# Kernel optimization log

Measured on AMD Instinct MI355X. Metric: run time of the kernel, lower is better.

Reference implementation:

```python
import jax, jax.numpy as jnp
import numpy as np

EPS = 1e-5

def conv(x, w, b, pad):
    y = jax.lax.conv_general_dilated(x, w, (1, 1), [(pad, pad), (pad, pad)],
                                     dimension_numbers=('NCHW', 'OIHW', 'NCHW'))
    return y + b[None, :, None, None]

def bn(x, g, be, m, v):
    return g[None, :, None, None] * (x - m[None, :, None, None]) * jax.lax.rsqrt(v[None, :, None, None] + EPS) + be[None, :, None, None]

def haar_dwt2(x):
    # pywt db1 dwt2 on even-sized images: per 2x2 block [[a,b],[c,d]]
    # cA=(a+b+c+d)/2, cH=(a+b-c-d)/2, cV=(a-b+c-d)/2, cD=(a-b-c+d)/2
    B, C, H, W = x.shape
    xr = x.reshape(B, C, H // 2, 2, W // 2, 2)
    a = xr[:, :, :, 0, :, 0]; b = xr[:, :, :, 0, :, 1]
    c = xr[:, :, :, 1, :, 0]; d = xr[:, :, :, 1, :, 1]
    cA = (a + b + c + d) * 0.5
    cH = (a + b - c - d) * 0.5
    cV = (a - b + c - d) * 0.5
    cD = (a - b - c + d) * 0.5
    return jnp.stack([cA, cH, cV, cD], axis=2)  # [B,C,4,H/2,W/2]

def setup_inputs() -> dict:
    key = jax.random.key(0)
    ks = iter(jax.random.split(key, 64))
    def w(shape, s=0.05):
        return jax.random.normal(next(ks), shape, dtype=jnp.float32) * s
    def vecs(c):  # gamma, beta, running_mean, running_var
        return (w((c,), 0.1) + 1.0, w((c,), 0.1), w((c,), 0.1),
                jax.random.uniform(next(ks), (c,), dtype=jnp.float32) + 0.5)
    inp = {'x': jax.random.normal(next(ks), (16, 3, 512, 512), dtype=jnp.float32)}
    inp['cw1'] = w((16, 3, 1, 1)); inp['cb1'] = w((16,))
    inp['cw2'] = w((3, 16, 1, 1)); inp['cb2'] = w((3,))
    inp['lw1'] = w((64, 3, 3, 3)); inp['lb1'] = w((64,))
    inp['lg1'], inp['lbe1'], inp['lm1'], inp['lv1'] = vecs(64)
    inp['lw2'] = w((128, 64, 3, 3)); inp['lb2'] = w((128,))
    inp['lg2'], inp['lbe2'], inp['lm2'], inp['lv2'] = vecs(128)
    inp['hw1'] = w((64, 9, 3, 3)); inp['hb1'] = w((64,))
    inp['hg1'], inp['hbe1'], inp['hm1'], inp['hv1'] = vecs(64)
    inp['hw2'] = w((128, 64, 3, 3)); inp['hb2'] = w((128,))
    inp['hg2'], inp['hbe2'], inp['hm2'], inp['hv2'] = vecs(128)
    inp['fw1'] = w((128, 256, 1, 1)); inp['fb1'] = w((128,))
    inp['fg1'], inp['fbe1'], inp['fm1'], inp['fv1'] = vecs(128)
    inp['fw2'] = w((64, 128, 1, 1)); inp['fb2'] = w((64,))
    inp['fg2'], inp['fbe2'], inp['fm2'], inp['fv2'] = vecs(64)
    return inp

def reference(x, cw1, cb1, cw2, cb2,
              lw1, lb1, lg1, lbe1, lm1, lv1, lw2, lb2, lg2, lbe2, lm2, lv2,
              hw1, hb1, hg1, hbe1, hm1, hv1, hw2, hb2, hg2, hbe2, hm2, hv2,
              fw1, fb1, fg1, fbe1, fm1, fv1, fw2, fb2, fg2, fbe2, fm2, fv2):
    hsv = conv(jax.nn.relu(conv(x, cw1, cb1, 0)), cw2, cb2, 0)
    coeffs = haar_dwt2(hsv)  # [B,3,4,H/2,W/2]
    B, C, _, H, W = coeffs.shape
    low = coeffs[:, :, 0]                                   # [B,3,H,W]
    high = coeffs[:, :, 1:].reshape(B, C * 3, H, W)         # [B,9,H,W]
    lf = jax.nn.relu(bn(conv(low, lw1, lb1, 1), lg1, lbe1, lm1, lv1))
    lf = jax.nn.relu(bn(conv(lf, lw2, lb2, 1), lg2, lbe2, lm2, lv2))
    hf = jax.nn.relu(bn(conv(high, hw1, hb1, 1), hg1, hbe1, hm1, hv1))
    hf = jax.nn.relu(bn(conv(hf, hw2, hb2, 1), hg2, hbe2, hm2, hv2))
    f = jnp.concatenate([lf, hf], axis=1)                   # [B,256,H,W]
    f = jax.nn.relu(bn(conv(f, fw1, fb1, 0), fg1, fbe1, fm1, fv1))
    f = jax.nn.relu(bn(conv(f, fw2, fb2, 0), fg2, fbe2, fm2, fv2))
    return f
```

## Files before the change

### kernel.cpp

```cpp
#include <hip/hip_runtime.h>
#include <hip/hip_bf16.h>


#define EPS_BN 1e-5f

typedef unsigned int u32;
typedef unsigned short u16;
typedef __attribute__((ext_vector_type(8))) short short8;
typedef __attribute__((ext_vector_type(4))) float f32x4;

__device__ __forceinline__ u16 f2bf(float f) {
  u32 u = __float_as_uint(f);
  u32 r = (u + 0x7fffu + ((u >> 16) & 1u)) >> 16;
  return (u16)r;
}

__global__ __launch_bounds__(256) void repack_kernel(
    const float* __restrict__ w, const float* __restrict__ bias,
    const float* __restrict__ g, const float* __restrict__ be,
    const float* __restrict__ m, const float* __restrict__ v,
    float* __restrict__ wrep, float* __restrict__ brep, int K, int COUT)
{
  int idx = blockIdx.x * 256 + threadIdx.x;
  if (idx < K * COUT) {
    int oc = idx % COUT;
    int k  = idx / COUT;
    float alpha = g[oc] * rsqrtf(v[oc] + EPS_BN);
    wrep[idx] = w[(size_t)oc * K + k] * alpha;
  }
  if (idx < COUT) {
    float alpha = g[idx] * rsqrtf(v[idx] + EPS_BN);
    brep[idx] = fmaf(bias[idx], alpha, be[idx] - m[idx] * alpha);
  }
}

__global__ __launch_bounds__(256) void repack_pack_kernel(
    const float* __restrict__ w, const float* __restrict__ bias,
    const float* __restrict__ g, const float* __restrict__ be,
    const float* __restrict__ m, const float* __restrict__ v,
    u16* __restrict__ wpk, float* __restrict__ brep,
    int CIN, int KHW, int COUT)
{
  int idx = blockIdx.x * 256 + threadIdx.x;
  int K = CIN * KHW * KHW;
  if (idx < K * COUT) {
    int oc = idx % COUT;
    int k  = idx / COUT;
    int ic = k % CIN;
    int kidx = k / CIN;
    int ky = kidx / KHW, kx = kidx % KHW;
    float alpha = g[oc] * rsqrtf(v[oc] + EPS_BN);
    float val = w[(((size_t)oc * CIN + ic) * KHW + ky) * KHW + kx] * alpha;
    int ks = k >> 5, c = (k >> 3) & 3, e = k & 7;
    wpk[((size_t)((ks * 4 + c) * COUT + oc)) * 8 + e] = f2bf(val);
  }
  if (idx < COUT) {
    float alpha = g[idx] * rsqrtf(v[idx] + EPS_BN);
    brep[idx] = fmaf(bias[idx], alpha, be[idx] - m[idx] * alpha);
  }
}

__global__ __launch_bounds__(256) void front_kernel(
    const float* __restrict__ x,
    const float* __restrict__ cw1, const float* __restrict__ cb1,
    const float* __restrict__ cw2, const float* __restrict__ cb2,
    float* __restrict__ low, float* __restrict__ high)
{
  const int pid = blockIdx.x * 256 + threadIdx.x;
  const int wo = pid & 255, ho = (pid >> 8) & 255, b = pid >> 16;
  float hsv[2][2][3];
  #pragma unroll
  for (int dy = 0; dy < 2; ++dy) {
    #pragma unroll
    for (int dx = 0; dx < 2; ++dx) {
      int h = 2 * ho + dy, w = 2 * wo + dx;
      size_t base = ((size_t)(b * 3) << 18) + (size_t)h * 512 + w;
      float p0 = x[base];
      float p1 = x[base + (1u << 18)];
      float p2 = x[base + (2u << 18)];
      float o0 = cb2[0], o1 = cb2[1], o2 = cb2[2];
      #pragma unroll
      for (int o = 0; o < 16; ++o) {
        float t = fmaf(cw1[o*3+2], p2, fmaf(cw1[o*3+1], p1, fmaf(cw1[o*3+0], p0, cb1[o])));
        t = fmaxf(t, 0.f);
        o0 = fmaf(cw2[o],      t, o0);
        o1 = fmaf(cw2[16 + o], t, o1);
        o2 = fmaf(cw2[32 + o], t, o2);
      }
      hsv[dy][dx][0] = o0; hsv[dy][dx][1] = o1; hsv[dy][dx][2] = o2;
    }
  }
  size_t lb = (size_t)pid * 3;
  size_t hb = (size_t)pid * 9;
  #pragma unroll
  for (int c = 0; c < 3; ++c) {
    float a  = hsv[0][0][c], bb = hsv[0][1][c];
    float cc = hsv[1][0][c], dd = hsv[1][1][c];
    low [lb + c]         = (a + bb + cc + dd) * 0.5f;
    high[hb + c*3 + 0]   = (a + bb - cc - dd) * 0.5f;
    high[hb + c*3 + 1]   = (a - bb + cc - dd) * 0.5f;
    high[hb + c*3 + 2]   = (a - bb - cc + dd) * 0.5f;
  }
}

template<int CIN, int COUT>
__global__ __launch_bounds__(256, 1) void conv3x3_bn_relu(
    const float* __restrict__ in_, const float* __restrict__ wrep,
    const float* __restrict__ brep, u16* __restrict__ out, int out_stride)
{
  __shared__ __align__(16) float tile[CIN * 18 * 19];
  const int tid = threadIdx.x;
  const int tx = tid & 15, ty = tid >> 4;
  const int w0 = blockIdx.x * 16, h0 = blockIdx.y * 16, b = blockIdx.z;

  for (int idx = tid; idx < 18 * 18 * CIN; idx += 256) {
    int ic = idx % CIN;
    int t  = idx / CIN;
    int x  = t % 18, y = t / 18;
    int gy = h0 + y - 1, gx = w0 + x - 1;
    bool ok = (gy >= 0 && gy < 256 && gx >= 0 && gx < 256);
    size_t gaddr = (size_t)((b * 256 + gy) * 256 + gx) * CIN + ic;
    tile[(ic * 18 + y) * 19 + x] = ok ? in_[gaddr] : 0.f;
  }
  __syncthreads();

  const size_t pix = (size_t)((b * 256 + (h0 + ty)) * 256 + (w0 + tx));
  constexpr int NG = COUT / 16;
  for (int gr = 0; gr < NG; ++gr) {
    float acc[16];
    #pragma unroll
    for (int j = 0; j < 16; ++j) acc[j] = 0.f;
    for (int ic = 0; ic < CIN; ++ic) {
      #pragma unroll
      for (int ky = 0; ky < 3; ++ky) {
        #pragma unroll
        for (int kx = 0; kx < 3; ++kx) {
          float a = tile[(ic * 18 + (ty + ky)) * 19 + (tx + kx)];
          const float* wp = wrep + (size_t)(ic * 9 + ky * 3 + kx) * COUT + gr * 16;
          #pragma unroll
          for (int j = 0; j < 16; ++j) acc[j] = fmaf(a, wp[j], acc[j]);
        }
      }
    }
    const float* bp = brep + gr * 16;
    size_t obase = pix * (size_t)out_stride + gr * 16;
    #pragma unroll
    for (int j = 0; j < 16; ++j) {
      float r = fmaxf(acc[j] + bp[j], 0.f);
      out[obase + j] = f2bf(r);
    }
  }
}

__global__ __launch_bounds__(256, 2) void conv3x3_mfma(
    const u16* __restrict__ in, const u16* __restrict__ wpk,
    const float* __restrict__ brep, u16* __restrict__ out,
    int out_stride, int out_choff)
{
  __shared__ __align__(16) unsigned char smem[3 * 8 * 132 * 16];
  uint4 (*Arow)[8][132] = (uint4(*)[8][132])smem;

  const int tid = threadIdx.x;
  const int l = tid & 63, wid = tid >> 6;
  const int bid = blockIdx.x;
  const int swz = (bid & 7) * 1024 + (bid >> 3);
  const int xh = swz & 1, h = (swz >> 1) & 255, b = swz >> 9;
  const int w0 = xh * 128;

  const int waveM = wid >> 1, waveN = wid & 1;
  const int pixW = waveM * 64, n0 = waveN * 64;
  const int lr = l & 15, lc = l >> 4;

  for (int i = tid; i < 3 * 130 * 8; i += 256) {
    int c = i & 7;
    int t = i >> 3;
    int px = t % 130;
    int row = t / 130;
    int gy = h + row - 1, gx = w0 + px - 1;
    uint4 vv = make_uint4(0, 0, 0, 0);
    if ((unsigned)gy < 256u && (unsigned)gx < 256u)
      vv = *(const uint4*)(in + ((size_t)((b * 256 + gy) * 256 + gx)) * 64 + c * 8);
    Arow[row][c][px] = vv;
  }
  __syncthreads();

  f32x4 acc[4][4];
  #pragma unroll
  for (int m = 0; m < 4; ++m)
    #pragma unroll
    for (int n = 0; n < 4; ++n)
      #pragma unroll
      for (int j = 0; j < 4; ++j) acc[m][n][j] = 0.f;

  const short8* wpk8 = (const short8*)wpk;
  #pragma unroll
  for (int kidx = 0; kidx < 9; ++kidx) {
    const int ky = kidx / 3, kx = kidx % 3;
    #pragma unroll
    for (int cs = 0; cs < 2; ++cs) {
      short8 a[4], bf[4];
      #pragma unroll
      for (int m = 0; m < 4; ++m)
        a[m] = *(const short8*)&Arow[ky][cs * 4 + lc][pixW + m * 16 + lr + kx];
      #pragma unroll
      for (int n = 0; n < 4; ++n)
        bf[n] = wpk8[((kidx * 2 + cs) * 4 + lc) * 128 + n0 + n * 16 + lr];
      #pragma unroll
      for (int m = 0; m < 4; ++m)
        #pragma unroll
        for (int n = 0; n < 4; ++n)
          acc[m][n] = __builtin_amdgcn_mfma_f32_16x16x32_bf16(a[m], bf[n], acc[m][n], 0, 0, 0);
    }
  }

  __syncthreads();
  u16 (*soutp)[136] = (u16(*)[136])smem;
  #pragma unroll
  for (int n = 0; n < 4; ++n) {
    const int oc = n0 + n * 16 + lr;
    const float bs = brep[oc];
    #pragma unroll
    for (int m = 0; m < 4; ++m)
      #pragma unroll
      for (int j = 0; j < 4; ++j)
        soutp[pixW + m * 16 + lc * 4 + j][oc] = f2bf(fmaxf(acc[m][n][j] + bs, 0.f));
  }
  __syncthreads();
  const size_t rowbase = (size_t)((b * 256 + h) * 256 + w0);
  for (int i = tid; i < 128 * 16; i += 256) {
    int c = i & 15, px = i >> 4;
    *(uint4*)(out + (rowbase + px) * (size_t)out_stride + out_choff + c * 8) =
        *(const uint4*)&soutp[px][c * 8];
  }
}

__global__ __launch_bounds__(256) void fuse_mfma(
    const u16* __restrict__ fcat,
    const u16* __restrict__ w1p, const float* __restrict__ b1r,
    const u16* __restrict__ w2p, const float* __restrict__ b2r,
    float* __restrict__ out)
{
  __shared__ __align__(16) unsigned char smem[8192 + 16 * 128 * 16];
  uint4 (*A_ld)[128] = (uint4(*)[128])smem;
  uint4 (*A2)[128]   = (uint4(*)[128])(smem + 8192);
  float (*sout)[132] = (float(*)[132])smem;

  const int tid = threadIdx.x;
  const int l = tid & 63, wid = tid >> 6;
  const int w0 = blockIdx.x * 128, hh = blockIdx.y, b = blockIdx.z;
  const int waveM = wid >> 1, waveN = wid & 1;
  const int pixW = waveM * 64, n0 = waveN * 64;
  const int lr = l & 15, lc = l >> 4;
  const int sp = tid & 127, cc = tid >> 7;
  const size_t rowbase = (size_t)((b * 256 + hh) * 256 + w0);

  f32x4 acc[4][4];
  #pragma unroll
  for (int m = 0; m < 4; ++m)
    #pragma unroll
    for (int n = 0; n < 4; ++n)
      #pragma unroll
      for (int j = 0; j < 4; ++j) acc[m][n][j] = 0.f;

  const short8* w1p8 = (const short8*)w1p;
  for (int ks = 0; ks < 8; ++ks) {
    const u16* src = fcat + (rowbase + sp) * 256 + ks * 32 + cc * 8;
    uint4 v0 = *(const uint4*)src;
    uint4 v1 = *(const uint4*)(src + 16);
    __syncthreads();
    A_ld[cc][sp] = v0;
    A_ld[cc + 2][sp] = v1;
    __syncthreads();
    short8 a[4], bf[4];
    #pragma unroll
    for (int m = 0; m < 4; ++m)
      a[m] = *(const short8*)&A_ld[lc][pixW + m * 16 + lr];
    #pragma unroll
    for (int n = 0; n < 4; ++n)
      bf[n] = w1p8[(ks * 4 + lc) * 128 + n0 + n * 16 + lr];
    #pragma unroll
    for (int m = 0; m < 4; ++m)
      #pragma unroll
      for (int n = 0; n < 4; ++n)
        acc[m][n] = __builtin_amdgcn_mfma_f32_16x16x32_bf16(a[m], bf[n], acc[m][n], 0, 0, 0);
  }

  u16* A2u = (u16*)A2;
  #pragma unroll
  for (int n = 0; n < 4; ++n) {
    const int oc = n0 + n * 16 + lr;
    const float bs = b1r[oc];
    #pragma unroll
    for (int m = 0; m < 4; ++m)
      #pragma unroll
      for (int j = 0; j < 4; ++j) {
        int px = pixW + m * 16 + lc * 4 + j;
        A2u[((size_t)(oc >> 3) * 128 + px) * 8 + (oc & 7)] =
            f2bf(fmaxf(acc[m][n][j] + bs, 0.f));
      }
  }
  __syncthreads();

  const int n02 = waveN * 32;
  f32x4 acc2[4][2];
  #pragma unroll
  for (int m = 0; m < 4; ++m)
    #pragma unroll
    for (int n = 0; n < 2; ++n)
      #pragma unroll
      for (int j = 0; j < 4; ++j) acc2[m][n][j] = 0.f;

  const short8* w2p8 = (const short8*)w2p;
  #pragma unroll
  for (int ks = 0; ks < 4; ++ks) {
    short8 a[4], bf[2];
    #pragma unroll
    for (int m = 0; m < 4; ++m)
      a[m] = *(const short8*)&A2[ks * 4 + lc][pixW + m * 16 + lr];
    #pragma unroll
    for (int n = 0; n < 2; ++n)
      bf[n] = w2p8[(ks * 4 + lc) * 64 + n02 + n * 16 + lr];
    #pragma unroll
    for (int m = 0; m < 4; ++m)
      #pragma unroll
      for (int n = 0; n < 2; ++n)
        acc2[m][n] = __builtin_amdgcn_mfma_f32_16x16x32_bf16(a[m], bf[n], acc2[m][n], 0, 0, 0);
  }
  __syncthreads();

  #pragma unroll
  for (int n = 0; n < 2; ++n) {
    const int oc = n02 + n * 16 + lr;
    const float bs = b2r[oc];
    #pragma unroll
    for (int m = 0; m < 4; ++m)
      #pragma unroll
      for (int j = 0; j < 4; ++j)
        sout[oc][pixW + m * 16 + lc * 4 + j] = fmaxf(acc2[m][n][j] + bs, 0.f);
  }
  __syncthreads();
  for (int i = tid; i < 64 * 128; i += 256) {
    int oc = i >> 7, px = i & 127;
    out[(((size_t)b * 64 + oc) << 16) + (size_t)hh * 256 + w0 + px] = sout[oc][px];
  }
}

extern "C" void kernel_launch(void* const* d_in, const int* in_sizes, int n_in,
                              void* d_out, int out_size, void* d_ws, size_t ws_size,
                              hipStream_t stream)
{
  const float* x   = (const float*)d_in[0];
  const float* cw1 = (const float*)d_in[1];
  const float* cb1 = (const float*)d_in[2];
  const float* cw2 = (const float*)d_in[3];
  const float* cb2 = (const float*)d_in[4];
  const float* lw1 = (const float*)d_in[5];
  const float* lb1 = (const float*)d_in[6];
  const float* lg1 = (const float*)d_in[7];
  const float* lbe1= (const float*)d_in[8];
  const float* lm1 = (const float*)d_in[9];
  const float* lv1 = (const float*)d_in[10];
  const float* lw2 = (const float*)d_in[11];
  const float* lb2 = (const float*)d_in[12];
  const float* lg2 = (const float*)d_in[13];
  const float* lbe2= (const float*)d_in[14];
  const float* lm2 = (const float*)d_in[15];
  const float* lv2 = (const float*)d_in[16];
  const float* hw1 = (const float*)d_in[17];
  const float* hb1 = (const float*)d_in[18];
  const float* hg1 = (const float*)d_in[19];
  const float* hbe1= (const float*)d_in[20];
  const float* hm1 = (const float*)d_in[21];
  const float* hv1 = (const float*)d_in[22];
  const float* hw2 = (const float*)d_in[23];
  const float* hb2 = (const float*)d_in[24];
  const float* hg2 = (const float*)d_in[25];
  const float* hbe2= (const float*)d_in[26];
  const float* hm2 = (const float*)d_in[27];
  const float* hv2 = (const float*)d_in[28];
  const float* fw1 = (const float*)d_in[29];
  const float* fb1 = (const float*)d_in[30];
  const float* fg1 = (const float*)d_in[31];
  const float* fbe1= (const float*)d_in[32];
  const float* fm1 = (const float*)d_in[33];
  const float* fv1 = (const float*)d_in[34];
  const float* fw2 = (const float*)d_in[35];
  const float* fb2 = (const float*)d_in[36];
  const float* fg2 = (const float*)d_in[37];
  const float* fbe2= (const float*)d_in[38];
  const float* fm2 = (const float*)d_in[39];
  const float* fv2 = (const float*)d_in[40];

  char* ws = (char*)d_ws;
  const size_t MB = 1024 * 1024;
  u16*   lf1  = (u16*)(ws);
  u16*   hf1  = (u16*)(ws + 135 * MB);
  char*  regA = ws + 270 * MB;
  float* low  = (float*)(regA);
  float* high = (float*)(regA + 13 * MB);
  u16*   fcat = (u16*)(regA);
  char*  wtail = regA + 538 * MB;
  size_t woff = 0;
  auto alloc = [&](size_t bytes) -> void* {
    void* p = wtail + woff;
    woff = (woff + bytes + 255) & ~(size_t)255;
    return p;
  };
  float* wl1r = (float*)alloc(27*64*4);     float* bl1r = (float*)alloc(64*4);
  float* wh1r = (float*)alloc(81*64*4);     float* bh1r = (float*)alloc(64*4);
  u16*   wl2p = (u16*)alloc(576*128*2);     float* bl2r = (float*)alloc(128*4);
  u16*   wh2p = (u16*)alloc(576*128*2);     float* bh2r = (float*)alloc(128*4);
  u16*   wf1p = (u16*)alloc(256*128*2);     float* bf1r = (float*)alloc(128*4);
  u16*   wf2p = (u16*)alloc(128*64*2);      float* bf2r = (float*)alloc(64*4);

  repack_kernel<<<(27*64+255)/256, 256, 0, stream>>>(lw1, lb1, lg1, lbe1, lm1, lv1, wl1r, bl1r, 27, 64);
  repack_kernel<<<(81*64+255)/256, 256, 0, stream>>>(hw1, hb1, hg1, hbe1, hm1, hv1, wh1r, bh1r, 81, 64);
  repack_pack_kernel<<<(576*128+255)/256, 256, 0, stream>>>(lw2, lb2, lg2, lbe2, lm2, lv2, wl2p, bl2r, 64, 3, 128);
  repack_pack_kernel<<<(576*128+255)/256, 256, 0, stream>>>(hw2, hb2, hg2, hbe2, hm2, hv2, wh2p, bh2r, 64, 3, 128);
  repack_pack_kernel<<<(256*128+255)/256, 256, 0, stream>>>(fw1, fb1, fg1, fbe1, fm1, fv1, wf1p, bf1r, 256, 1, 128);
  repack_pack_kernel<<<(128*64+255)/256,  256, 0, stream>>>(fw2, fb2, fg2, fbe2, fm2, fv2, wf2p, bf2r, 128, 1, 64);

  front_kernel<<<4096, 256, 0, stream>>>(x, cw1, cb1, cw2, cb2, low, high);

  dim3 cgrid(16, 16, 16);
  conv3x3_bn_relu<3, 64><<<cgrid, 256, 0, stream>>>(low,  wl1r, bl1r, lf1, 64);
  conv3x3_bn_relu<9, 64><<<cgrid, 256, 0, stream>>>(high, wh1r, bh1r, hf1, 64);

  conv3x3_mfma<<<8192, 256, 0, stream>>>(lf1, wl2p, bl2r, fcat, 256, 0);
  conv3x3_mfma<<<8192, 256, 0, stream>>>(hf1, wh2p, bh2r, fcat, 256, 128);

  dim3 fgrid(2, 256, 16);
  fuse_mfma<<<fgrid, 256, 0, stream>>>(fcat, wf1p, bf1r, wf2p, bf2r, (float*)d_out);
}
```

Baseline: 1.193 ms.

## Move first-stage 3x3 convs to bf16 MFMA and retile fused 1x1 stage

The first-layer 3x3 convolutions (3 and 9 input channels) now run on MFMA bf16 matrix instructions instead of scalar fp32 FMA loops. To make that possible, the front kernel writes low/high bands as bf16 records zero-padded to 16 channels, and weights are packed with zero padding to 160 K. The fused 1x1 kernel now stages the whole 64-pixel row tile into LDS once, with padded stride and two blocks per CU, instead of syncing per K-step. The second conv also gets an extra LDS padding column against bank conflicts. Costs: bf16 rounding of the first-layer inputs and wasted MFMA work on the padded channels.

Result: faster. 1.050 ms (-12.0%).

```diff
diff --git a/kernel.cpp b/kernel.cpp
--- a/kernel.cpp
+++ b/kernel.cpp
@@ -13,25 +13,6 @@
   u32 u = __float_as_uint(f);
   u32 r = (u + 0x7fffu + ((u >> 16) & 1u)) >> 16;
   return (u16)r;
-}
-
-__global__ __launch_bounds__(256) void repack_kernel(
-    const float* __restrict__ w, const float* __restrict__ bias,
-    const float* __restrict__ g, const float* __restrict__ be,
-    const float* __restrict__ m, const float* __restrict__ v,
-    float* __restrict__ wrep, float* __restrict__ brep, int K, int COUT)
-{
-  int idx = blockIdx.x * 256 + threadIdx.x;
-  if (idx < K * COUT) {
-    int oc = idx % COUT;
-    int k  = idx / COUT;
-    float alpha = g[oc] * rsqrtf(v[oc] + EPS_BN);
-    wrep[idx] = w[(size_t)oc * K + k] * alpha;
-  }
-  if (idx < COUT) {
-    float alpha = g[idx] * rsqrtf(v[idx] + EPS_BN);
-    brep[idx] = fmaf(bias[idx], alpha, be[idx] - m[idx] * alpha);
-  }
 }
 
 __global__ __launch_bounds__(256) void repack_pack_kernel(
@@ -60,11 +41,37 @@
   }
 }
 
+__global__ __launch_bounds__(256) void repack_pad_pack_kernel(
+    const float* __restrict__ w, const float* __restrict__ bias,
+    const float* __restrict__ g, const float* __restrict__ be,
+    const float* __restrict__ m, const float* __restrict__ v,
+    u16* __restrict__ wpk, float* __restrict__ brep, int CIN, int COUT)
+{
+  int idx = blockIdx.x * 256 + threadIdx.x;
+  if (idx < 160 * COUT) {
+    int oc = idx % COUT;
+    int k  = idx / COUT;
+    int kidx = k >> 4, ic = k & 15;
+    float val = 0.f;
+    if (kidx < 9 && ic < CIN) {
+      int ky = kidx / 3, kx = kidx % 3;
+      float alpha = g[oc] * rsqrtf(v[oc] + EPS_BN);
+      val = w[(((size_t)oc * CIN + ic) * 3 + ky) * 3 + kx] * alpha;
+    }
+    int ks = k >> 5, c = (k >> 3) & 3, e = k & 7;
+    wpk[((size_t)((ks * 4 + c) * COUT + oc)) * 8 + e] = f2bf(val);
+  }
+  if (idx < COUT) {
+    float alpha = g[idx] * rsqrtf(v[idx] + EPS_BN);
+    brep[idx] = fmaf(bias[idx], alpha, be[idx] - m[idx] * alpha);
+  }
+}
+
 __global__ __launch_bounds__(256) void front_kernel(
     const float* __restrict__ x,
     const float* __restrict__ cw1, const float* __restrict__ cb1,
     const float* __restrict__ cw2, const float* __restrict__ cb2,
-    float* __restrict__ low, float* __restrict__ high)
+    u16* __restrict__ low16, u16* __restrict__ high16)
 {
   const int pid = blockIdx.x * 256 + threadIdx.x;
   const int wo = pid & 255, ho = (pid >> 8) & 255, b = pid >> 16;
@@ -90,65 +97,97 @@
       hsv[dy][dx][0] = o0; hsv[dy][dx][1] = o1; hsv[dy][dx][2] = o2;
     }
   }
-  size_t lb = (size_t)pid * 3;
-  size_t hb = (size_t)pid * 9;
+  u16 lrec[16], hrec[16];
+  #pragma unroll
+  for (int i = 0; i < 16; ++i) { lrec[i] = 0; hrec[i] = 0; }
   #pragma unroll
   for (int c = 0; c < 3; ++c) {
     float a  = hsv[0][0][c], bb = hsv[0][1][c];
     float cc = hsv[1][0][c], dd = hsv[1][1][c];
-    low [lb + c]         = (a + bb + cc + dd) * 0.5f;
-    high[hb + c*3 + 0]   = (a + bb - cc - dd) * 0.5f;
-    high[hb + c*3 + 1]   = (a - bb + cc - dd) * 0.5f;
-    high[hb + c*3 + 2]   = (a - bb - cc + dd) * 0.5f;
-  }
-}
-
-template<int CIN, int COUT>
-__global__ __launch_bounds__(256, 1) void conv3x3_bn_relu(
-    const float* __restrict__ in_, const float* __restrict__ wrep,
-    const float* __restrict__ brep, u16* __restrict__ out, int out_stride)
-{
-  __shared__ __align__(16) float tile[CIN * 18 * 19];
+    lrec[c]         = f2bf((a + bb + cc + dd) * 0.5f);
+    hrec[c * 3 + 0] = f2bf((a + bb - cc - dd) * 0.5f);
+    hrec[c * 3 + 1] = f2bf((a - bb + cc - dd) * 0.5f);
+    hrec[c * 3 + 2] = f2bf((a - bb - cc + dd) * 0.5f);
+  }
+  *(uint4*)(low16  + (size_t)pid * 16)     = *(const uint4*)&lrec[0];
+  *(uint4*)(low16  + (size_t)pid * 16 + 8) = *(const uint4*)&lrec[8];
+  *(uint4*)(high16 + (size_t)pid * 16)     = *(const uint4*)&hrec[0];
+  *(uint4*)(high16 + (size_t)pid * 16 + 8) = *(const uint4*)&hrec[8];
+}
+
+__global__ __launch_bounds__(256) void conv3x3s_mfma(
+    const u16* __restrict__ in16, const u16* __restrict__ wpk,
+    const float* __restrict__ brep, u16* __restrict__ out)
+{
+  __shared__ __align__(16) u16 smem[3 * 130 * 24];
+  u16 (*Arow)[130][24] = (u16(*)[130][24])smem;
+
   const int tid = threadIdx.x;
-  const int tx = tid & 15, ty = tid >> 4;
-  const int w0 = blockIdx.x * 16, h0 = blockIdx.y * 16, b = blockIdx.z;
-
-  for (int idx = tid; idx < 18 * 18 * CIN; idx += 256) {
-    int ic = idx % CIN;
-    int t  = idx / CIN;
-    int x  = t % 18, y = t / 18;
-    int gy = h0 + y - 1, gx = w0 + x - 1;
-    bool ok = (gy >= 0 && gy < 256 && gx >= 0 && gx < 256);
-    size_t gaddr = (size_t)((b * 256 + gy) * 256 + gx) * CIN + ic;
-    tile[(ic * 18 + y) * 19 + x] = ok ? in_[gaddr] : 0.f;
-  }
-  __syncthreads();
-
-  const size_t pix = (size_t)((b * 256 + (h0 + ty)) * 256 + (w0 + tx));
-  constexpr int NG = COUT / 16;
-  for (int gr = 0; gr < NG; ++gr) {
-    float acc[16];
-    #pragma unroll
-    for (int j = 0; j < 16; ++j) acc[j] = 0.f;
-    for (int ic = 0; ic < CIN; ++ic) {
-      #pragma unroll
-      for (int ky = 0; ky < 3; ++ky) {
-        #pragma unroll
-        for (int kx = 0; kx < 3; ++kx) {
-          float a = tile[(ic * 18 + (ty + ky)) * 19 + (tx + kx)];
-          const float* wp = wrep + (size_t)(ic * 9 + ky * 3 + kx) * COUT + gr * 16;
-          #pragma unroll
-          for (int j = 0; j < 16; ++j) acc[j] = fmaf(a, wp[j], acc[j]);
-        }
-      }
-    }
-    const float* bp = brep + gr * 16;
-    size_t obase = pix * (size_t)out_stride + gr * 16;
-    #pragma unroll
-    for (int j = 0; j < 16; ++j) {
-      float r = fmaxf(acc[j] + bp[j], 0.f);
-      out[obase + j] = f2bf(r);
-    }
+  const int l = tid & 63, wid = tid >> 6;
+  const int bid = blockIdx.x;
+  const int swz = (bid & 7) * 1024 + (bid >> 3);
+  const int xh = swz & 1, h = (swz >> 1) & 255, b = swz >> 9;
+  const int w0 = xh * 128;
+  const int pixW = (wid >> 1) * 64, n0 = (wid & 1) * 32;
+  const int lr = l & 15, lc = l >> 4;
+
+  for (int i = tid; i < 3 * 130 * 2; i += 256) {
+    int half = i & 1, rec = i >> 1;
+    int px = rec % 130, row = rec / 130;
+    int gy = h + row - 1, gx = w0 + px - 1;
+    uint4 vv = make_uint4(0, 0, 0, 0);
+    if ((unsigned)gy < 256u && (unsigned)gx < 256u)
+      vv = *(const uint4*)(in16 + ((size_t)((b * 256 + gy) * 256 + gx)) * 16 + half * 8);
+    *(uint4*)&Arow[row][px][half * 8] = vv;
+  }
+  __syncthreads();
+
+  f32x4 acc[4][2];
+  #pragma unroll
+  for (int m = 0; m < 4; ++m)
+    #pragma unroll
+    for (int n = 0; n < 2; ++n)
+      #pragma unroll
+      for (int j = 0; j < 4; ++j) acc[m][n][j] = 0.f;
+
+  const short8* wpk8 = (const short8*)wpk;
+  #pragma unroll
+  for (int s = 0; s < 5; ++s) {
+    int kidx = s * 2 + (lc >> 1);
+    int ky = (kidx < 9) ? (kidx / 3) : 0;
+    int kx = (kidx < 9) ? (kidx % 3) : 0;
+    int chb = (lc & 1) * 8;
+    short8 a[4], bf[2];
+    #pragma unroll
+    for (int m = 0; m < 4; ++m)
+      a[m] = *(const short8*)&Arow[ky][pixW + m * 16 + lr + kx][chb];
+    #pragma unroll
+    for (int n = 0; n < 2; ++n)
+      bf[n] = wpk8[(s * 4 + lc) * 64 + n0 + n * 16 + lr];
+    #pragma unroll
+    for (int m = 0; m < 4; ++m)
+      #pragma unroll
+      for (int n = 0; n < 2; ++n)
+        acc[m][n] = __builtin_amdgcn_mfma_f32_16x16x32_bf16(a[m], bf[n], acc[m][n], 0, 0, 0);
+  }
+
+  __syncthreads();
+  u16 (*soutp)[72] = (u16(*)[72])smem;
+  #pragma unroll
+  for (int n = 0; n < 2; ++n) {
+    const int oc = n0 + n * 16 + lr;
+    const float bs = brep[oc];
+    #pragma unroll
+    for (int m = 0; m < 4; ++m)
+      #pragma unroll
+      for (int j = 0; j < 4; ++j)
+        soutp[pixW + m * 16 + lc * 4 + j][oc] = f2bf(fmaxf(acc[m][n][j] + bs, 0.f));
+  }
+  __syncthreads();
+  const size_t rowbase = (size_t)((b * 256 + h) * 256 + w0);
+  for (int i = tid; i < 128 * 8; i += 256) {
+    int c = i & 7, px = i >> 3;
+    *(uint4*)(out + (rowbase + px) * 64 + c * 8) = *(const uint4*)&soutp[px][c * 8];
   }
 }
 
@@ -157,8 +196,8 @@
     const float* __restrict__ brep, u16* __restrict__ out,
     int out_stride, int out_choff)
 {
-  __shared__ __align__(16) unsigned char smem[3 * 8 * 132 * 16];
-  uint4 (*Arow)[8][132] = (uint4(*)[8][132])smem;
+  __shared__ __align__(16) unsigned char smem[3 * 8 * 133 * 16];
+  uint4 (*Arow)[8][133] = (uint4(*)[8][133])smem;
 
   const int tid = threadIdx.x;
   const int l = tid & 63, wid = tid >> 6;
@@ -234,77 +273,75 @@
   }
 }
 
-__global__ __launch_bounds__(256) void fuse_mfma(
+__global__ __launch_bounds__(256, 2) void fuse_mfma(
     const u16* __restrict__ fcat,
     const u16* __restrict__ w1p, const float* __restrict__ b1r,
     const u16* __restrict__ w2p, const float* __restrict__ b2r,
     float* __restrict__ out)
 {
-  __shared__ __align__(16) unsigned char smem[8192 + 16 * 128 * 16];
-  uint4 (*A_ld)[128] = (uint4(*)[128])smem;
-  uint4 (*A2)[128]   = (uint4(*)[128])(smem + 8192);
-  float (*sout)[132] = (float(*)[132])smem;
-
+  __shared__ __align__(16) uint4 smem4[32 * 65];
   const int tid = threadIdx.x;
   const int l = tid & 63, wid = tid >> 6;
-  const int w0 = blockIdx.x * 128, hh = blockIdx.y, b = blockIdx.z;
-  const int waveM = wid >> 1, waveN = wid & 1;
-  const int pixW = waveM * 64, n0 = waveN * 64;
+  const int w0 = blockIdx.x * 64, hh = blockIdx.y, b = blockIdx.z;
+  const int pixW = (wid >> 1) * 32;
+  const int n0 = (wid & 1) * 64;
   const int lr = l & 15, lc = l >> 4;
-  const int sp = tid & 127, cc = tid >> 7;
   const size_t rowbase = (size_t)((b * 256 + hh) * 256 + w0);
 
-  f32x4 acc[4][4];
-  #pragma unroll
-  for (int m = 0; m < 4; ++m)
+  #pragma unroll
+  for (int it = 0; it < 8; ++it) {
+    int i = it * 256 + tid;
+    int px = i >> 5, c = i & 31;
+    smem4[c * 65 + px] = *(const uint4*)(fcat + (rowbase + px) * 256 + c * 8);
+  }
+  __syncthreads();
+
+  f32x4 acc[2][4];
+  #pragma unroll
+  for (int m = 0; m < 2; ++m)
     #pragma unroll
     for (int n = 0; n < 4; ++n)
       #pragma unroll
       for (int j = 0; j < 4; ++j) acc[m][n][j] = 0.f;
 
   const short8* w1p8 = (const short8*)w1p;
+  #pragma unroll
   for (int ks = 0; ks < 8; ++ks) {
-    const u16* src = fcat + (rowbase + sp) * 256 + ks * 32 + cc * 8;
-    uint4 v0 = *(const uint4*)src;
-    uint4 v1 = *(const uint4*)(src + 16);
-    __syncthreads();
-    A_ld[cc][sp] = v0;
-    A_ld[cc + 2][sp] = v1;
-    __syncthreads();
-    short8 a[4], bf[4];
-    #pragma unroll
-    for (int m = 0; m < 4; ++m)
-      a[m] = *(const short8*)&A_ld[lc][pixW + m * 16 + lr];
+    short8 a[2], bf[4];
+    #pragma unroll
+    for (int m = 0; m < 2; ++m)
+      a[m] = *(const short8*)&smem4[(ks * 4 + lc) * 65 + pixW + m * 16 + lr];
     #pragma unroll
     for (int n = 0; n < 4; ++n)
       bf[n] = w1p8[(ks * 4 + lc) * 128 + n0 + n * 16 + lr];
     #pragma unroll
-    for (int m = 0; m < 4; ++m)
+    for (int m = 0; m < 2; ++m)
       #pragma unroll
       for (int n = 0; n < 4; ++n)
         acc[m][n] = __builtin_amdgcn_mfma_f32_16x16x32_bf16(a[m], bf[n], acc[m][n], 0, 0, 0);
   }
-
-  u16* A2u = (u16*)A2;
+  __syncthreads();
+
+  u16* A2u = (u16*)smem4;
   #pragma unroll
   for (int n = 0; n < 4; ++n) {
     const int oc = n0 + n * 16 + lr;
     const float bs = b1r[oc];
     #pragma unroll
-    for (int m = 0; m < 4; ++m)
+    for (int m = 0; m < 2; ++m)
       #pragma unroll
       for (int j = 0; j < 4; ++j) {
         int px = pixW + m * 16 + lc * 4 + j;
-        A2u[((size_t)(oc >> 3) * 128 + px) * 8 + (oc & 7)] =
+        A2u[((size_t)(oc >> 3) * 65 + px) * 8 + (oc & 7)] =
             f2bf(fmaxf(acc[m][n][j] + bs, 0.f));
       }
   }
   __syncthreads();
 
-  const int n02 = waveN * 32;
-  f32x4 acc2[4][2];
-  #pragma unroll
-  for (int m = 0; m < 4; ++m)
+  const int n02 = (wid & 1) * 32;
+  f32x4 acc2[2][2];
+  #pragma unroll
+  for (int m = 0; m < 2; ++m)
     #pragma unroll
     for (int n = 0; n < 2; ++n)
       #pragma unroll
@@ -313,34 +350,35 @@
   const short8* w2p8 = (const short8*)w2p;
   #pragma unroll
   for (int ks = 0; ks < 4; ++ks) {
-    short8 a[4], bf[2];
-    #pragma unroll
-    for (int m = 0; m < 4; ++m)
-      a[m] = *(const short8*)&A2[ks * 4 + lc][pixW + m * 16 + lr];
+    short8 a[2], bf[2];
+    #pragma unroll
+    for (int m = 0; m < 2; ++m)
+      a[m] = *(const short8*)&smem4[(ks * 4 + lc) * 65 + pixW + m * 16 + lr];
     #pragma unroll
     for (int n = 0; n < 2; ++n)
       bf[n] = w2p8[(ks * 4 + lc) * 64 + n02 + n * 16 + lr];
     #pragma unroll
-    for (int m = 0; m < 4; ++m)
+    for (int m = 0; m < 2; ++m)
       #pragma unroll
       for (int n = 0; n < 2; ++n)
         acc2[m][n] = __builtin_amdgcn_mfma_f32_16x16x32_bf16(a[m], bf[n], acc2[m][n], 0, 0, 0);
   }
   __syncthreads();
 
+  float (*sout)[65] = (float(*)[65])smem4;
   #pragma unroll
   for (int n = 0; n < 2; ++n) {
     const int oc = n02 + n * 16 + lr;
     const float bs = b2r[oc];
     #pragma unroll
-    for (int m = 0; m < 4; ++m)
+    for (int m = 0; m < 2; ++m)
       #pragma unroll
       for (int j = 0; j < 4; ++j)
         sout[oc][pixW + m * 16 + lc * 4 + j] = fmaxf(acc2[m][n][j] + bs, 0.f);
   }
   __syncthreads();
-  for (int i = tid; i < 64 * 128; i += 256) {
-    int oc = i >> 7, px = i & 127;
+  for (int i = tid; i < 64 * 64; i += 256) {
+    int oc = i >> 6, px = i & 63;
     out[(((size_t)b * 64 + oc) << 16) + (size_t)hh * 256 + w0 + px] = sout[oc][px];
   }
 }
@@ -393,42 +431,41 @@
 
   char* ws = (char*)d_ws;
   const size_t MB = 1024 * 1024;
-  u16*   lf1  = (u16*)(ws);
-  u16*   hf1  = (u16*)(ws + 135 * MB);
-  char*  regA = ws + 270 * MB;
-  float* low  = (float*)(regA);
-  float* high = (float*)(regA + 13 * MB);
-  u16*   fcat = (u16*)(regA);
-  char*  wtail = regA + 538 * MB;
+  u16* lf1    = (u16*)(ws);
+  u16* hf1    = (u16*)(ws + 135 * MB);
+  char* regA  = ws + 270 * MB;
+  u16* low16  = (u16*)(regA);
+  u16* high16 = (u16*)(regA + 34 * MB);
+  u16* fcat   = (u16*)(regA);
+  char* wtail = regA + 538 * MB;
   size_t woff = 0;
   auto alloc = [&](size_t bytes) -> void* {
     void* p = wtail + woff;
     woff = (woff + bytes + 255) & ~(size_t)255;
     return p;
   };
-  float* wl1r = (float*)alloc(27*64*4);     float* bl1r = (float*)alloc(64*4);
-  float* wh1r = (float*)alloc(81*64*4);     float* bh1r = (float*)alloc(64*4);
-  u16*   wl2p = (u16*)alloc(576*128*2);     float* bl2r = (float*)alloc(128*4);
-  u16*   wh2p = (u16*)alloc(576*128*2);     float* bh2r = (float*)alloc(128*4);
-  u16*   wf1p = (u16*)alloc(256*128*2);     float* bf1r = (float*)alloc(128*4);
-  u16*   wf2p = (u16*)alloc(128*64*2);      float* bf2r = (float*)alloc(64*4);
-
-  repack_kernel<<<(27*64+255)/256, 256, 0, stream>>>(lw1, lb1, lg1, lbe1, lm1, lv1, wl1r, bl1r, 27, 64);
-  repack_kernel<<<(81*64+255)/256, 256, 0, stream>>>(hw1, hb1, hg1, hbe1, hm1, hv1, wh1r, bh1r, 81, 64);
+  u16* wl1p = (u16*)alloc(160*64*2);    float* bl1r = (float*)alloc(64*4);
+  u16* wh1p = (u16*)alloc(160*64*2);    float* bh1r = (float*)alloc(64*4);
+  u16* wl2p = (u16*)alloc(576*128*2);   float* bl2r = (float*)alloc(128*4);
+  u16* wh2p = (u16*)alloc(576*128*2);   float* bh2r = (float*)alloc(128*4);
+  u16* wf1p = (u16*)alloc(256*128*2);   float* bf1r = (float*)alloc(128*4);
+  u16* wf2p = (u16*)alloc(128*64*2);    float* bf2r = (float*)alloc(64*4);
+
+  repack_pad_pack_kernel<<<40, 256, 0, stream>>>(lw1, lb1, lg1, lbe1, lm1, lv1, wl1p, bl1r, 3, 64);
+  repack_pad_pack_kernel<<<40, 256, 0, stream>>>(hw1, hb1, hg1, hbe1, hm1, hv1, wh1p, bh1r, 9, 64);
   repack_pack_kernel<<<(576*128+255)/256, 256, 0, stream>>>(lw2, lb2, lg2, lbe2, lm2, lv2, wl2p, bl2r, 64, 3, 128);
   repack_pack_kernel<<<(576*128+255)/256, 256, 0, stream>>>(hw2, hb2, hg2, hbe2, hm2, hv2, wh2p, bh2r, 64, 3, 128);
   repack_pack_kernel<<<(256*128+255)/256, 256, 0, stream>>>(fw1, fb1, fg1, fbe1, fm1, fv1, wf1p, bf1r, 256, 1, 128);
   repack_pack_kernel<<<(128*64+255)/256,  256, 0, stream>>>(fw2, fb2, fg2, fbe2, fm2, fv2, wf2p, bf2r, 128, 1, 64);
 
-  front_kernel<<<4096, 256, 0, stream>>>(x, cw1, cb1, cw2, cb2, low, high);
-
-  dim3 cgrid(16, 16, 16);
-  conv3x3_bn_relu<3, 64><<<cgrid, 256, 0, stream>>>(low,  wl1r, bl1r, lf1, 64);
-  conv3x3_bn_relu<9, 64><<<cgrid, 256, 0, stream>>>(high, wh1r, bh1r, hf1, 64);
+  front_kernel<<<4096, 256, 0, stream>>>(x, cw1, cb1, cw2, cb2, low16, high16);
+
+  conv3x3s_mfma<<<8192, 256, 0, stream>>>(low16,  wl1p, bl1r, lf1);
+  conv3x3s_mfma<<<8192, 256, 0, stream>>>(high16, wh1p, bh1r, hf1);
 
   conv3x3_mfma<<<8192, 256, 0, stream>>>(lf1, wl2p, bl2r, fcat, 256, 0);
   conv3x3_mfma<<<8192, 256, 0, stream>>>(hf1, wh2p, bh2r, fcat, 256, 128);
 
-  dim3 fgrid(2, 256, 16);
+  dim3 fgrid(4, 256, 16);
   fuse_mfma<<<fgrid, 256, 0, stream>>>(fcat, wf1p, bf1r, wf2p, bf2r, (float*)d_out);
 }
```
